# Performance work log

Hardware: AMD Instinct MI355X
Metric: run time of the kernel (lower is better)

The kernel has to match this reference:

```python
import math
import jax, jax.numpy as jnp
import numpy as np

B, S, M, H = 8, 2048, 2048, 512
GH = 512  # gate_hidden
MIX_BIAS = -0.25
VARIATION_BIAS = -1.0
PRIOR_SCALE = 1.0
GATE_SCALE = 1.0
GATE_BIAS = 0.0
EPS = 1e-6


def _slerp(a, b, t, eps=EPS):
    # F.normalize semantics: x / max(||x||, eps)
    an = a / jnp.maximum(jnp.linalg.norm(a, axis=-1, keepdims=True), eps)
    bn = b / jnp.maximum(jnp.linalg.norm(b, axis=-1, keepdims=True), eps)
    dot = jnp.clip(jnp.sum(an * bn, axis=-1, keepdims=True), -1.0 + eps, 1.0 - eps)
    omega = jnp.arccos(dot)
    sin_omega = jnp.maximum(jnp.sin(omega), eps)
    t = jnp.clip(t, 0.0, 1.0)
    scale_a = jnp.sin((1.0 - t) * omega) / sin_omega
    scale_b = jnp.sin(t * omega) / sin_omega
    return scale_a * a + scale_b * b


def setup_inputs() -> dict:
    key = jax.random.key(0)
    ks = jax.random.split(key, 20)
    sc = 1.0 / math.sqrt(H)
    sc4 = 1.0 / math.sqrt(4 * H)
    scg = 1.0 / math.sqrt(GH)
    inp = {
        "query": jax.random.normal(ks[0], (B, S, H), jnp.float32),
        "global_anchor": jax.random.normal(ks[1], (B, H), jnp.float32),
        "global_memory": jax.random.normal(ks[2], (B, M, H), jnp.float32),
        "local_absolute": jax.random.normal(ks[3], (B, S, H), jnp.float32),
        "style_context": jax.random.normal(ks[4], (B, S, H), jnp.float32),
        # projection params, stored as [in, out]
        "Wq": jax.random.normal(ks[5], (H, H), jnp.float32) * sc,
        "bq": jnp.zeros((H,), jnp.float32),
        "Wk": jax.random.normal(ks[6], (H, H), jnp.float32) * sc,
        "bk": jnp.zeros((H,), jnp.float32),
        "Wv": jax.random.normal(ks[7], (H, H), jnp.float32) * sc,
        "bv": jnp.zeros((H,), jnp.float32),
        "Wo": jax.random.normal(ks[8], (H, H), jnp.float32) * sc,
        "bo": jnp.zeros((H,), jnp.float32),
        # mix gate MLP: 4H -> GH -> 1
        "Wm1": jax.random.normal(ks[9], (4 * H, GH), jnp.float32) * sc4,
        "bm1": jnp.zeros((GH,), jnp.float32),
        "Wm2": jax.random.normal(ks[10], (GH, 1), jnp.float32) * scg,
        "bm2": jnp.zeros((1,), jnp.float32),
        # variation gate MLP: 4H -> GH -> 1
        "Wg1": jax.random.normal(ks[11], (4 * H, GH), jnp.float32) * sc4,
        "bg1": jnp.zeros((GH,), jnp.float32),
        "Wg2": jax.random.normal(ks[12], (GH, 1), jnp.float32) * scg,
        "bg2": jnp.zeros((1,), jnp.float32),
    }
    return inp


def reference(query, global_anchor, global_memory, local_absolute, style_context,
              Wq, bq, Wk, bk, Wv, bv, Wo, bo,
              Wm1, bm1, Wm2, bm2, Wg1, bg1, Wg2, bg2):
    # expand anchor [B,H] -> [B,S,H]
    anchor_seq = jnp.broadcast_to(global_anchor[:, None, :], query.shape)

    q = query @ Wq + bq                      # [B,S,H]
    k = global_memory @ Wk + bk              # [B,M,H]
    v = global_memory @ Wv + bv              # [B,M,H]

    attn_logits = jnp.einsum('bsh,bmh->bsm', q, k) / math.sqrt(float(H))
    attn = jax.nn.softmax(attn_logits, axis=-1)                      # [B,S,M]
    prior_delta = (jnp.einsum('bsm,bmh->bsh', attn, v) @ Wo + bo) * PRIOR_SCALE
    prior_absolute = anchor_seq + prior_delta

    mix_in = jnp.concatenate([query, prior_absolute, local_absolute, style_context], axis=-1)
    mix_logit = jax.nn.relu(mix_in @ Wm1 + bm1) @ Wm2 + bm2          # [B,S,1]
    mix = jax.nn.sigmoid(mix_logit + MIX_BIAS)

    candidate_absolute = _slerp(prior_absolute, local_absolute, mix)

    var_in = jnp.concatenate([query, candidate_absolute, anchor_seq, style_context], axis=-1)
    variation_logit = jax.nn.relu(var_in @ Wg1 + bg1) @ Wg2 + bg2    # [B,S,1]
    variation_gate = jax.nn.sigmoid(variation_logit * GATE_SCALE + GATE_BIAS + VARIATION_BIAS)

    candidate_delta = candidate_absolute - anchor_seq
    return (attn, prior_delta, prior_absolute, mix, candidate_absolute,
            candidate_delta, variation_logit, variation_gate)
```

## Files before the change

kernel.cpp:

```cpp
#include <hip/hip_runtime.h>
#include <hip/hip_bf16.h>

typedef __hip_bfloat16 bf16;
typedef unsigned short u16;
typedef u16 u16x8 __attribute__((ext_vector_type(8)));
typedef u16 u16x4v __attribute__((ext_vector_type(4)));
typedef short bf16x8 __attribute__((ext_vector_type(8)));
typedef float f32x4 __attribute__((ext_vector_type(4)));

__device__ __forceinline__ float b2f(u16 u) {
    unsigned v = ((unsigned)u) << 16;
    float f; __builtin_memcpy(&f, &v, 4); return f;
}
__device__ __forceinline__ u16 f2u(float f) {
    bf16 h = __float2bfloat16(f);
    u16 u; __builtin_memcpy(&u, &h, 2); return u;
}
__device__ __forceinline__ float sigmoidf_(float x) { return 1.f / (1.f + expf(-x)); }
__device__ __forceinline__ void load8f(const float* __restrict__ p, float* x) {
    float4 a = *reinterpret_cast<const float4*>(p);
    float4 b = *reinterpret_cast<const float4*>(p + 4);
    x[0]=a.x; x[1]=a.y; x[2]=a.z; x[3]=a.w; x[4]=b.x; x[5]=b.y; x[6]=b.z; x[7]=b.w;
}

__device__ __forceinline__ void gld16(const void* g, void* l) {
    typedef __attribute__((address_space(1))) const unsigned int GU;
    typedef __attribute__((address_space(3))) unsigned int LU;
    __builtin_amdgcn_global_load_lds((GU*)(unsigned long long)g,
                                     (LU*)(unsigned int)(unsigned long long)l, 16, 0, 0);
}

template<int EPI>
__global__ __launch_bounds__(256)
void k_mfma(const bf16* __restrict__ A, long long sA, int lda,
            const bf16* __restrict__ Bt, long long sB, int ldb,
            const float* __restrict__ bias,
            bf16* __restrict__ outb, long long sO,
            float* __restrict__ out1, float* __restrict__ out2,
            const float* __restrict__ anchor,
            int N, int K, float scale)
{
    __shared__ short As[4096];
    __shared__ short Bs[4096];
    const int tid = threadIdx.x;
    const int z = blockIdx.z;
    const int n0 = blockIdx.x * 128, m0 = blockIdx.y * 128;
    const bf16* Az = A + (long long)z * sA;
    const bf16* Bz = Bt + (long long)z * sB;
    const int lrow = tid >> 2;
    const int lcol = (tid & 3) * 8;
    const int lane = tid & 63, w = tid >> 6;
    const int wm = (w >> 1) * 64, wn = (w & 1) * 64;
    const int fr = lane & 15, fq = lane >> 4;
    char* AsW = (char*)As + w * 1024;
    char* BsW = (char*)Bs + w * 1024;

    f32x4 acc[4][4];
#pragma unroll
    for (int i = 0; i < 4; ++i)
#pragma unroll
        for (int j = 0; j < 4; ++j) acc[i][j] = f32x4{0.f, 0.f, 0.f, 0.f};

    for (int k0 = 0; k0 < K; k0 += 32) {
        const bf16* ga = Az + (long long)(m0 + lrow) * lda + (k0 + lcol);
        const bf16* gb = Bz + (long long)(n0 + lrow) * ldb + (k0 + lcol);
        gld16(ga, AsW);
        gld16(ga + 64LL * lda, AsW + 4096);
        gld16(gb, BsW);
        gld16(gb + 64LL * ldb, BsW + 4096);
        __syncthreads();

        bf16x8 af[4], bfr[4];
#pragma unroll
        for (int i = 0; i < 4; ++i)
            af[i] = *reinterpret_cast<const bf16x8*>(&As[(wm + i * 16 + fr) * 32 + fq * 8]);
#pragma unroll
        for (int j = 0; j < 4; ++j)
            bfr[j] = *reinterpret_cast<const bf16x8*>(&Bs[(wn + j * 16 + fr) * 32 + fq * 8]);
#pragma unroll
        for (int i = 0; i < 4; ++i)
#pragma unroll
            for (int j = 0; j < 4; ++j)
                acc[i][j] = __builtin_amdgcn_mfma_f32_16x16x32_bf16(af[i], bfr[j], acc[i][j], 0, 0, 0);
        __syncthreads();
    }

#pragma unroll
    for (int j = 0; j < 4; ++j) {
        const int col = n0 + wn + j * 16 + fr;
        const float bv = bias ? bias[col] : 0.f;
#pragma unroll
        for (int i = 0; i < 4; ++i) {
#pragma unroll
            for (int r = 0; r < 4; ++r) {
                const long long row = m0 + wm + i * 16 + fq * 4 + r;
                const float v = acc[i][j][r];
                if constexpr (EPI == 0) {
                    outb[(long long)z * sO + row * N + col] = __float2bfloat16(v * scale + bv);
                } else if constexpr (EPI == 2) {
                    const float pd = v + bv;
                    const float pa = pd + anchor[(row >> 11) * 512 + col];
                    out1[row * N + col] = pd;
                    out2[row * N + col] = pa;
                    outb[row * N + col] = __float2bfloat16(pa);
                } else {
                    outb[(row >> 11) * 1048576LL + (long long)col * 2048 + (row & 2047)]
                        = __float2bfloat16(v + bv);
                }
            }
        }
    }
}

__global__ __launch_bounds__(256)
void k_softmax_b(bf16* __restrict__ Lb, float* __restrict__ attn)
{
    __shared__ float redm[4], reds[4];
    const long long row = blockIdx.x;
    bf16* lp = Lb + row * 2048;
    float* ap = attn + row * 2048;
    const int tid = threadIdx.x;

    u16x8 u = *reinterpret_cast<const u16x8*>(lp + tid * 8);
    float x[8];
    float mx = -1e30f;
#pragma unroll
    for (int j = 0; j < 8; ++j) { x[j] = b2f(u[j]); mx = fmaxf(mx, x[j]); }
#pragma unroll
    for (int off = 32; off; off >>= 1) mx = fmaxf(mx, __shfl_xor(mx, off));
    if ((tid & 63) == 0) redm[tid >> 6] = mx;
    __syncthreads();
    mx = fmaxf(fmaxf(redm[0], redm[1]), fmaxf(redm[2], redm[3]));

    float s = 0.f;
#pragma unroll
    for (int j = 0; j < 8; ++j) { x[j] = __expf(x[j] - mx); s += x[j]; }
#pragma unroll
    for (int off = 32; off; off >>= 1) s += __shfl_xor(s, off);
    if ((tid & 63) == 0) reds[tid >> 6] = s;
    __syncthreads();
    const float inv = 1.f / (reds[0] + reds[1] + reds[2] + reds[3]);

    u16x8 ob;
#pragma unroll
    for (int j = 0; j < 8; ++j) { x[j] *= inv; ob[j] = f2u(x[j]); }
    *reinterpret_cast<float4*>(ap + tid * 8)     = make_float4(x[0], x[1], x[2], x[3]);
    *reinterpret_cast<float4*>(ap + tid * 8 + 4) = make_float4(x[4], x[5], x[6], x[7]);
    *reinterpret_cast<u16x8*>(lp + tid * 8) = ob;
}

__global__ __launch_bounds__(256)
void k_cat(const bf16* __restrict__ s0b, const bf16* __restrict__ s1b,
           const bf16* __restrict__ s2b, const bf16* __restrict__ s3b,
           int mode2,
           const bf16* __restrict__ Bt, const float* __restrict__ bias,
           bf16* __restrict__ outb)
{
    __shared__ short As[4096];
    __shared__ short Bs[4096];
    const int tid = threadIdx.x;
    const int n0 = blockIdx.x * 128, m0 = blockIdx.y * 128;
    const int lrow = tid >> 2;
    const int lcol = (tid & 3) * 8;
    const int lane = tid & 63, w = tid >> 6;
    const int wm = (w >> 1) * 64, wn = (w & 1) * 64;
    const int fr = lane & 15, fq = lane >> 4;
    char* AsW = (char*)As + w * 1024;
    char* BsW = (char*)Bs + w * 1024;

    f32x4 acc[4][4];
#pragma unroll
    for (int i = 0; i < 4; ++i)
#pragma unroll
        for (int j = 0; j < 4; ++j) acc[i][j] = f32x4{0.f, 0.f, 0.f, 0.f};

    for (int k0 = 0; k0 < 2048; k0 += 32) {
        const int si = k0 >> 9;
        const bf16* sp = si == 0 ? s0b : si == 1 ? s1b : si == 2 ? s2b : s3b;
        const int kloc = (k0 & 511) + lcol;
        const int r = m0 + lrow;
        long long ro0, ro1;
        if (si == 2 && mode2) { ro0 = (long long)(r >> 11) * 512; ro1 = ro0; }
        else                  { ro0 = (long long)r * 512; ro1 = ro0 + 64LL * 512; }
        gld16(sp + ro0 + kloc, AsW);
        gld16(sp + ro1 + kloc, AsW + 4096);
        const bf16* gb = Bt + (long long)(n0 + lrow) * 2048 + (k0 + lcol);
        gld16(gb, BsW);
        gld16(gb + 64LL * 2048, BsW + 4096);
        __syncthreads();

        bf16x8 af[4], bfr[4];
#pragma unroll
        for (int i = 0; i < 4; ++i)
            af[i] = *reinterpret_cast<const bf16x8*>(&As[(wm + i * 16 + fr) * 32 + fq * 8]);
#pragma unroll
        for (int j = 0; j < 4; ++j)
            bfr[j] = *reinterpret_cast<const bf16x8*>(&Bs[(wn + j * 16 + fr) * 32 + fq * 8]);
#pragma unroll
        for (int i = 0; i < 4; ++i)
#pragma unroll
            for (int j = 0; j < 4; ++j)
                acc[i][j] = __builtin_amdgcn_mfma_f32_16x16x32_bf16(af[i], bfr[j], acc[i][j], 0, 0, 0);
        __syncthreads();
    }

#pragma unroll
    for (int j = 0; j < 4; ++j) {
        const int col = n0 + wn + j * 16 + fr;
        const float bv = bias[col];
#pragma unroll
        for (int i = 0; i < 4; ++i)
#pragma unroll
            for (int r = 0; r < 4; ++r) {
                const long long row = m0 + wm + i * 16 + fq * 4 + r;
                outb[row * 512 + col] = __float2bfloat16(fmaxf(acc[i][j][r] + bv, 0.f));
            }
    }
}

__global__ __launch_bounds__(256)
void k_cvt(const float* __restrict__ s, bf16* __restrict__ d, int n)
{
    long long i = ((long long)blockIdx.x * 256 + threadIdx.x) * 8;
    if (i >= n) return;
    float x[8]; load8f(s + i, x);
    u16x8 o;
#pragma unroll
    for (int j = 0; j < 8; ++j) o[j] = f2u(x[j]);
    *reinterpret_cast<u16x8*>(d + i) = o;
}

__global__ __launch_bounds__(256)
void k_tr(const float* s0, bf16* d0, const float* s1, bf16* d1,
          const float* s2, bf16* d2, const float* s3, bf16* d3,
          int R, int C)
{
    __shared__ float t[32][33];
    const int zz = blockIdx.z;
    const float* s = zz == 0 ? s0 : zz == 1 ? s1 : zz == 2 ? s2 : s3;
    bf16* d = zz == 0 ? d0 : zz == 1 ? d1 : zz == 2 ? d2 : d3;
    const int c0 = blockIdx.x * 32, r0 = blockIdx.y * 32;
    const int tr = threadIdx.x >> 3, tc = (threadIdx.x & 7) * 4;
    float4 v = *reinterpret_cast<const float4*>(s + (long long)(r0 + tr) * C + c0 + tc);
    t[tr][tc] = v.x; t[tr][tc + 1] = v.y; t[tr][tc + 2] = v.z; t[tr][tc + 3] = v.w;
    __syncthreads();
    u16x4v o;
    o[0] = f2u(t[tc + 0][tr]); o[1] = f2u(t[tc + 1][tr]);
    o[2] = f2u(t[tc + 2][tr]); o[3] = f2u(t[tc + 3][tr]);
    *reinterpret_cast<u16x4v*>(d + (long long)(c0 + tr) * R + r0 + tc) = o;
}

__global__ __launch_bounds__(64)
void k_gate(const bf16* __restrict__ hidden, const float* __restrict__ w2,
            const float* __restrict__ b2,
            float* __restrict__ outLogit, float* __restrict__ outGate,
            float scl, float add)
{
    const long long row = blockIdx.x;
    const int lane = threadIdx.x;
    u16x8 u = *reinterpret_cast<const u16x8*>(hidden + row * 512 + lane * 8);
    float wv[8];
    load8f(w2 + lane * 8, wv);
    float s = 0.f;
#pragma unroll
    for (int j = 0; j < 8; ++j) s = fmaf(b2f(u[j]), wv[j], s);
#pragma unroll
    for (int off = 32; off; off >>= 1) s += __shfl_xor(s, off);
    if (lane == 0) {
        float logit = s + b2[0];
        if (outLogit) outLogit[row] = logit;
        outGate[row] = sigmoidf_(logit * scl + add);
    }
}

__global__ __launch_bounds__(64)
void k_slerp(const bf16* __restrict__ priorb, const bf16* __restrict__ localb,
             const float* __restrict__ mixv, const float* __restrict__ anchor,
             float* __restrict__ cand, float* __restrict__ cdelta,
             bf16* __restrict__ candb)
{
    const int row = blockIdx.x;
    const int lane = threadIdx.x;
    const long long base = (long long)row * 512 + lane * 8;
    const long long abase = (long long)(row >> 11) * 512 + lane * 8;

    u16x8 ua = *reinterpret_cast<const u16x8*>(priorb + base);
    u16x8 ub = *reinterpret_cast<const u16x8*>(localb + base);
    float a[8], b[8];
    float sa = 0.f, sb = 0.f, sab = 0.f;
#pragma unroll
    for (int j = 0; j < 8; ++j) {
        a[j] = b2f(ua[j]); b[j] = b2f(ub[j]);
        sa = fmaf(a[j], a[j], sa); sb = fmaf(b[j], b[j], sb); sab = fmaf(a[j], b[j], sab);
    }
#pragma unroll
    for (int off = 1; off < 64; off <<= 1) {
        sa += __shfl_xor(sa, off); sb += __shfl_xor(sb, off); sab += __shfl_xor(sab, off);
    }
    const float eps = 1e-6f;
    float na = fmaxf(sqrtf(sa), eps), nb = fmaxf(sqrtf(sb), eps);
    float dot = sab / (na * nb);
    dot = fminf(fmaxf(dot, -1.f + eps), 1.f - eps);
    float omega = acosf(dot);
    float so = fmaxf(sinf(omega), eps);
    float t = mixv[row];
    t = fminf(fmaxf(t, 0.f), 1.f);
    float sca = sinf((1.f - t) * omega) / so;
    float scb = sinf(t * omega) / so;

    float an[8];
    load8f(anchor + abase, an);
    float c0[8], d0[8];
    u16x8 cb;
#pragma unroll
    for (int j = 0; j < 8; ++j) {
        c0[j] = sca * a[j] + scb * b[j];
        d0[j] = c0[j] - an[j];
        cb[j] = f2u(c0[j]);
    }
    *reinterpret_cast<float4*>(cand + base)       = make_float4(c0[0], c0[1], c0[2], c0[3]);
    *reinterpret_cast<float4*>(cand + base + 4)   = make_float4(c0[4], c0[5], c0[6], c0[7]);
    *reinterpret_cast<float4*>(cdelta + base)     = make_float4(d0[0], d0[1], d0[2], d0[3]);
    *reinterpret_cast<float4*>(cdelta + base + 4) = make_float4(d0[4], d0[5], d0[6], d0[7]);
    *reinterpret_cast<u16x8*>(candb + base) = cb;
}

extern "C" void kernel_launch(void* const* d_in, const int* in_sizes, int n_in,
                              void* d_out, int out_size, void* d_ws, size_t ws_size,
                              hipStream_t stream)
{
    const float* query  = (const float*)d_in[0];
    const float* anchor = (const float*)d_in[1];
    const float* gmem   = (const float*)d_in[2];
    const float* local_ = (const float*)d_in[3];
    const float* style  = (const float*)d_in[4];
    const float* Wq = (const float*)d_in[5];   const float* bq = (const float*)d_in[6];
    const float* Wk = (const float*)d_in[7];   const float* bk = (const float*)d_in[8];
    const float* Wv = (const float*)d_in[9];   const float* bv = (const float*)d_in[10];
    const float* Wo = (const float*)d_in[11];  const float* bo = (const float*)d_in[12];
    const float* Wm1 = (const float*)d_in[13]; const float* bm1 = (const float*)d_in[14];
    const float* Wm2 = (const float*)d_in[15]; const float* bm2 = (const float*)d_in[16];
    const float* Wg1 = (const float*)d_in[17]; const float* bg1 = (const float*)d_in[18];
    const float* Wg2 = (const float*)d_in[19]; const float* bg2 = (const float*)d_in[20];

    float* out = (float*)d_out;
    const long long SHE = 8388608LL;
    float* o_attn = out;
    float* o_pd   = out + 33554432LL;
    float* o_pa   = o_pd + SHE;
    float* o_mix  = o_pa + SHE;
    float* o_ca   = o_mix + 16384;
    float* o_cd   = o_ca + SHE;
    float* o_vl   = o_cd + SHE;
    float* o_vg   = o_vl + 16384;

    bf16* S0q = (bf16*)d_ws;
    bf16* S1  = S0q + SHE;
    bf16* S2  = S1 + SHE;
    bf16* S3  = S2 + SHE;
    bf16* S4  = S3 + SHE;
    bf16* wtq = S4 + SHE;
    bf16* wtk = wtq + 262144;
    bf16* wtv = wtk + 262144;
    bf16* wto = wtv + 262144;
    bf16* wtm1 = wto + 262144;
    bf16* wtg1 = wtm1 + 1048576;
    bf16* anb  = wtg1 + 1048576;
    bf16* p_b  = (bf16*)o_ca;

    const float invSqrtH = 0.04419417382415922f;

    k_cvt<<<4096, 256, 0, stream>>>(query, S0q, 8388608);
    k_cvt<<<4096, 256, 0, stream>>>(gmem, S1, 8388608);
    k_cvt<<<2, 256, 0, stream>>>(anchor, anb, 4096);
    k_tr<<<dim3(16, 16, 4), 256, 0, stream>>>(Wq, wtq, Wk, wtk, Wv, wtv, Wo, wto, 512, 512);
    k_tr<<<dim3(16, 64, 2), 256, 0, stream>>>(Wm1, wtm1, Wg1, wtg1,
                                              nullptr, nullptr, nullptr, nullptr, 2048, 512);
    k_mfma<0><<<dim3(4, 128, 1), 256, 0, stream>>>(S0q, 0, 512, wtq, 0, 512, bq,
        S2, 0, nullptr, nullptr, nullptr, 512, 512, 1.f);
    k_mfma<0><<<dim3(4, 128, 1), 256, 0, stream>>>(S1, 0, 512, wtk, 0, 512, bk,
        S3, 0, nullptr, nullptr, nullptr, 512, 512, 1.f);
    k_mfma<3><<<dim3(4, 128, 1), 256, 0, stream>>>(S1, 0, 512, wtv, 0, 512, bv,
        S4, 0, nullptr, nullptr, nullptr, 512, 512, 1.f);
    k_mfma<0><<<dim3(16, 16, 8), 256, 0, stream>>>(S2, 2048LL * 512, 512, S3, 2048LL * 512, 512,
        nullptr, p_b, 4194304LL, nullptr, nullptr, nullptr, 2048, 512, invSqrtH);
    k_softmax_b<<<16384, 256, 0, stream>>>(p_b, o_attn);
    k_mfma<0><<<dim3(4, 16, 8), 256, 0, stream>>>(p_b, 4194304LL, 2048, S4, 1048576LL, 2048,
        nullptr, S1, 1048576LL, nullptr, nullptr, nullptr, 512, 2048, 1.f);
    k_cvt<<<4096, 256, 0, stream>>>(local_, S3, 8388608);
    k_cvt<<<4096, 256, 0, stream>>>(style, S4, 8388608);
    k_mfma<2><<<dim3(4, 128, 1), 256, 0, stream>>>(S1, 0, 512, wto, 0, 512, bo,
        S2, 0, o_pd, o_pa, anchor, 512, 512, 1.f);
    k_cat<<<dim3(4, 128, 1), 256, 0, stream>>>(S0q, S2, S3, S4, 0, wtm1, bm1, S1);
    k_gate<<<16384, 64, 0, stream>>>(S1, Wm2, bm2, nullptr, o_mix, 1.0f, -0.25f);
    k_slerp<<<16384, 64, 0, stream>>>(S2, S3, o_mix, anchor, o_ca, o_cd, S2);
    k_cat<<<dim3(4, 128, 1), 256, 0, stream>>>(S0q, S2, anb, S4, 1, wtg1, bg1, S1);
    k_gate<<<16384, 64, 0, stream>>>(S1, Wg2, bg2, o_vl, o_vg, 1.0f, -1.0f);
}
```

Measured before the change: 481.1 us.

## Remap GEMM blocks across XCDs and transpose V with a separate coalesced kernel

```diff
diff --git a/kernel.cpp b/kernel.cpp
--- a/kernel.cpp
+++ b/kernel.cpp
@@ -30,7 +30,7 @@
                                      (LU*)(unsigned int)(unsigned long long)l, 16, 0, 0);
 }
 
-template<int EPI>
+template<int EPI, int SWZ>
 __global__ __launch_bounds__(256)
 void k_mfma(const bf16* __restrict__ A, long long sA, int lda,
             const bf16* __restrict__ Bt, long long sB, int ldb,
@@ -38,13 +38,21 @@
             bf16* __restrict__ outb, long long sO,
             float* __restrict__ out1, float* __restrict__ out2,
             const float* __restrict__ anchor,
-            int N, int K, float scale)
+            int N, int K, float scale, int GX)
 {
     __shared__ short As[4096];
     __shared__ short Bs[4096];
     const int tid = threadIdx.x;
-    const int z = blockIdx.z;
-    const int n0 = blockIdx.x * 128, m0 = blockIdx.y * 128;
+    const int lin = blockIdx.x;
+    int x, y, z;
+    if constexpr (SWZ == 0) {
+        z = lin & 7; const int t = lin >> 3; x = t % GX; y = t / GX;
+    } else {
+        const int q = (int)gridDim.x >> 3;
+        const int wq = (lin & 7) * q + (lin >> 3);
+        x = wq % GX; y = wq / GX; z = 0;
+    }
+    const int n0 = x * 128, m0 = y * 128;
     const bf16* Az = A + (long long)z * sA;
     const bf16* Bz = Bt + (long long)z * sB;
     const int lrow = tid >> 2;
@@ -97,15 +105,12 @@
                 const float v = acc[i][j][r];
                 if constexpr (EPI == 0) {
                     outb[(long long)z * sO + row * N + col] = __float2bfloat16(v * scale + bv);
-                } else if constexpr (EPI == 2) {
+                } else {
                     const float pd = v + bv;
                     const float pa = pd + anchor[(row >> 11) * 512 + col];
                     out1[row * N + col] = pd;
                     out2[row * N + col] = pa;
                     outb[row * N + col] = __float2bfloat16(pa);
-                } else {
-                    outb[(row >> 11) * 1048576LL + (long long)col * 2048 + (row & 2047)]
-                        = __float2bfloat16(v + bv);
                 }
             }
         }
@@ -159,7 +164,10 @@
     __shared__ short As[4096];
     __shared__ short Bs[4096];
     const int tid = threadIdx.x;
-    const int n0 = blockIdx.x * 128, m0 = blockIdx.y * 128;
+    const int lin = blockIdx.x;
+    const int q = (int)gridDim.x >> 3;
+    const int wq = (lin & 7) * q + (lin >> 3);
+    const int n0 = (wq & 3) * 128, m0 = (wq >> 2) * 128;
     const int lrow = tid >> 2;
     const int lcol = (tid & 3) * 8;
     const int lane = tid & 63, w = tid >> 6;
@@ -250,6 +258,23 @@
     *reinterpret_cast<u16x4v*>(d + (long long)(c0 + tr) * R + r0 + tc) = o;
 }
 
+__global__ __launch_bounds__(256)
+void k_trb(const bf16* __restrict__ vb, bf16* __restrict__ vt)
+{
+    __shared__ u16 t[32][36];
+    const int z = blockIdx.z;
+    const int h0 = blockIdx.x * 32, s0 = blockIdx.y * 32;
+    const int tr = threadIdx.x >> 3, tc = (threadIdx.x & 7) * 4;
+    u16x4v a = *reinterpret_cast<const u16x4v*>(
+        vb + ((long long)z * 2048 + s0 + tr) * 512 + h0 + tc);
+    t[tr][tc] = a[0]; t[tr][tc + 1] = a[1]; t[tr][tc + 2] = a[2]; t[tr][tc + 3] = a[3];
+    __syncthreads();
+    u16x4v o;
+    o[0] = t[tc + 0][tr]; o[1] = t[tc + 1][tr]; o[2] = t[tc + 2][tr]; o[3] = t[tc + 3][tr];
+    *reinterpret_cast<u16x4v*>(
+        vt + (long long)z * 1048576 + (long long)(h0 + tr) * 2048 + s0 + tc) = o;
+}
+
 __global__ __launch_bounds__(64)
 void k_gate(const bf16* __restrict__ hidden, const float* __restrict__ w2,
             const float* __restrict__ b2,
@@ -367,6 +392,7 @@
     bf16* wtg1 = wtm1 + 1048576;
     bf16* anb  = wtg1 + 1048576;
     bf16* p_b  = (bf16*)o_ca;
+    bf16* v_b  = (bf16*)o_ca;
 
     const float invSqrtH = 0.04419417382415922f;
 
@@ -376,24 +402,25 @@
     k_tr<<<dim3(16, 16, 4), 256, 0, stream>>>(Wq, wtq, Wk, wtk, Wv, wtv, Wo, wto, 512, 512);
     k_tr<<<dim3(16, 64, 2), 256, 0, stream>>>(Wm1, wtm1, Wg1, wtg1,
                                               nullptr, nullptr, nullptr, nullptr, 2048, 512);
-    k_mfma<0><<<dim3(4, 128, 1), 256, 0, stream>>>(S0q, 0, 512, wtq, 0, 512, bq,
-        S2, 0, nullptr, nullptr, nullptr, 512, 512, 1.f);
-    k_mfma<0><<<dim3(4, 128, 1), 256, 0, stream>>>(S1, 0, 512, wtk, 0, 512, bk,
-        S3, 0, nullptr, nullptr, nullptr, 512, 512, 1.f);
-    k_mfma<3><<<dim3(4, 128, 1), 256, 0, stream>>>(S1, 0, 512, wtv, 0, 512, bv,
-        S4, 0, nullptr, nullptr, nullptr, 512, 512, 1.f);
-    k_mfma<0><<<dim3(16, 16, 8), 256, 0, stream>>>(S2, 2048LL * 512, 512, S3, 2048LL * 512, 512,
-        nullptr, p_b, 4194304LL, nullptr, nullptr, nullptr, 2048, 512, invSqrtH);
+    k_mfma<0, 1><<<512, 256, 0, stream>>>(S0q, 0, 512, wtq, 0, 512, bq,
+        S2, 0, nullptr, nullptr, nullptr, 512, 512, 1.f, 4);
+    k_mfma<0, 1><<<512, 256, 0, stream>>>(S1, 0, 512, wtk, 0, 512, bk,
+        S3, 0, nullptr, nullptr, nullptr, 512, 512, 1.f, 4);
+    k_mfma<0, 1><<<512, 256, 0, stream>>>(S1, 0, 512, wtv, 0, 512, bv,
+        v_b, 0, nullptr, nullptr, nullptr, 512, 512, 1.f, 4);
+    k_trb<<<dim3(16, 64, 8), 256, 0, stream>>>(v_b, S4);
+    k_mfma<0, 0><<<2048, 256, 0, stream>>>(S2, 2048LL * 512, 512, S3, 2048LL * 512, 512,
+        nullptr, p_b, 4194304LL, nullptr, nullptr, nullptr, 2048, 512, invSqrtH, 16);
     k_softmax_b<<<16384, 256, 0, stream>>>(p_b, o_attn);
-    k_mfma<0><<<dim3(4, 16, 8), 256, 0, stream>>>(p_b, 4194304LL, 2048, S4, 1048576LL, 2048,
-        nullptr, S1, 1048576LL, nullptr, nullptr, nullptr, 512, 2048, 1.f);
+    k_mfma<0, 0><<<512, 256, 0, stream>>>(p_b, 4194304LL, 2048, S4, 1048576LL, 2048,
+        nullptr, S1, 1048576LL, nullptr, nullptr, nullptr, 512, 2048, 1.f, 4);
     k_cvt<<<4096, 256, 0, stream>>>(local_, S3, 8388608);
     k_cvt<<<4096, 256, 0, stream>>>(style, S4, 8388608);
-    k_mfma<2><<<dim3(4, 128, 1), 256, 0, stream>>>(S1, 0, 512, wto, 0, 512, bo,
-        S2, 0, o_pd, o_pa, anchor, 512, 512, 1.f);
-    k_cat<<<dim3(4, 128, 1), 256, 0, stream>>>(S0q, S2, S3, S4, 0, wtm1, bm1, S1);
+    k_mfma<2, 1><<<512, 256, 0, stream>>>(S1, 0, 512, wto, 0, 512, bo,
+        S2, 0, o_pd, o_pa, anchor, 512, 512, 1.f, 4);
+    k_cat<<<512, 256, 0, stream>>>(S0q, S2, S3, S4, 0, wtm1, bm1, S1);
     k_gate<<<16384, 64, 0, stream>>>(S1, Wm2, bm2, nullptr, o_mix, 1.0f, -0.25f);
     k_slerp<<<16384, 64, 0, stream>>>(S2, S3, o_mix, anchor, o_ca, o_cd, S2);
-    k_cat<<<dim3(4, 128, 1), 256, 0, stream>>>(S0q, S2, anb, S4, 1, wtg1, bg1, S1);
+    k_cat<<<512, 256, 0, stream>>>(S0q, S2, anb, S4, 1, wtg1, bg1, S1);
     k_gate<<<16384, 64, 0, stream>>>(S1, Wg2, bg2, o_vl, o_vg, 1.0f, -1.0f);
 }
```

Measured after the change: 459.4 us. -4.5%, faster.
